# Performance work log

Hardware: AMD Instinct MI355X
Metric: run time of the kernel (lower is better)

## Reference

```python
import jax, jax.numpy as jnp
import numpy as np

N_NODES = 100000    # nodes in river network
N_PATHS = 1000000   # number of (src, dst) routing paths
MAX_DELAY = 16
DT = 1.0
CASCADE = 1.0
T = int(MAX_DELAY / DT)        # expanded time window (assert in original)
E = 8000000                    # total flattened path-node entries


def setup_inputs() -> dict:
    key = jax.random.key(0)
    k1, k2, k3 = jax.random.split(key, 3)
    params = jax.random.uniform(k1, (N_NODES,), dtype=jnp.float32)
    path_idxs = jnp.sort(jax.random.randint(k2, (E,), 0, N_PATHS, dtype=jnp.int32))
    path_nodes = jax.random.randint(k3, (E,), 0, N_NODES, dtype=jnp.int32)
    return {"params": params, "path_idxs": path_idxs, "path_nodes": path_nodes}


def reference(params, path_idxs, path_nodes):
    # irf_fn 'linear_storage': per-node linear-reservoir impulse response h(t)=exp(-t/k)/k
    k = params + 0.5                                  # storage const in [0.5, 1.5)
    t = jnp.arange(T, dtype=params.dtype) * DT        # [T]
    irfs = jnp.exp(-t[None, :] / k[:, None]) / k[:, None]   # [N, T]
    # frequency domain
    irfs_freq = jnp.fft.rfft(irfs, n=T, axis=-1)      # [N, F] complex
    # irf_agg 'log_triton': cascade-combine IRFs along each path = product of
    # transfer functions, done in log domain: gather logs, segment-sum per path.
    log_freq = jnp.log(irfs_freq)                     # [N, F] complex log
    gathered = log_freq[path_nodes]                   # [E, F] irregular gather
    agg_re = jax.ops.segment_sum(gathered.real, path_idxs, num_segments=N_PATHS)
    agg_im = jax.ops.segment_sum(gathered.imag, path_idxs, num_segments=N_PATHS)
    agg_log = (agg_re + 1j * agg_im) * CASCADE        # [P, F]
    irfs_freq_agg = jnp.exp(agg_log)
    # back to time domain
    irfs_agg = jnp.fft.irfft(irfs_freq_agg, n=T, axis=-1)   # [P, T]
    irfs_agg = jax.nn.relu(irfs_agg)
    irfs_agg = jnp.flip(irfs_agg, -1)                 # sampler.phi_k is identity for dt=1
    irfs_agg = irfs_agg / jnp.sum(irfs_agg, -1, keepdims=True)
    return irfs_agg                                   # COO values; coords scatter is a storage step
```

## Files before the change

### kernel.cpp

```cpp
#include <hip/hip_runtime.h>
#include <math.h>

#define N_NODES  100000
#define N_PATHS  1000000
#define E_TOT    8000000
#define NW_TOT   (E_TOT / 4)
#define NF       9
#define TAB_U32  25000
#define EB       1024
#define EPT      8
#define PB       256
#define KW       9

#define RMIN 0.135330f
#define RMAX 0.513420f
#define QSCALE (255.0f / (RMAX - RMIN))
#define DEQ    ((RMAX - RMIN) / 255.0f)

typedef int   v4i __attribute__((ext_vector_type(4)));
typedef float v4f __attribute__((ext_vector_type(4)));

__device__ __constant__ float COS16[16] = {
  1.0f,  0.92387953f,  0.70710678f,  0.38268343f,  0.0f, -0.38268343f, -0.70710678f, -0.92387953f,
 -1.0f, -0.92387953f, -0.70710678f, -0.38268343f,  0.0f,  0.38268343f,  0.70710678f,  0.92387953f };
__device__ __constant__ float SIN16[16] = {
  0.0f,  0.38268343f,  0.70710678f,  0.92387953f,  1.0f,  0.92387953f,  0.70710678f,  0.38268343f,
  0.0f, -0.38268343f, -0.70710678f, -0.92387953f, -1.0f, -0.92387953f, -0.70710678f, -0.38268343f };

__global__ void node_rq_kernel(const float* __restrict__ params,
                               unsigned char* __restrict__ rtab_q) {
    int n = blockIdx.x * blockDim.x + threadIdx.x;
    if (n >= N_NODES) return;
    float k = params[n] + 0.5f;
    float r = expf(-1.0f / k);
    float q = (r - RMIN) * QSCALE;
    q = fminf(fmaxf(q + 0.5f, 0.0f), 255.0f);
    rtab_q[n] = (unsigned char)q;
}

__device__ __forceinline__ void put_bounds(int a, int b, int e, int* __restrict__ start) {
    for (int p = a + 1; p <= b; ++p) start[p] = e;
}

__global__ __launch_bounds__(EB) void epass_kernel(const int* __restrict__ pidx,
                                                   const int* __restrict__ pnode,
                                                   const unsigned int* __restrict__ rtab_q,
                                                   int* __restrict__ start,
                                                   unsigned char* __restrict__ r8_all) {
    __shared__ unsigned int tab[TAB_U32];
    const unsigned char* tabb = (const unsigned char*)tab;
    int tid = threadIdx.x;
    for (int i = tid; i < TAB_U32; i += EB) tab[i] = rtab_q[i];
    __syncthreads();

    int base_q = blockIdx.x * EB * EPT;
#pragma unroll
    for (int g = 0; g < EPT; g++) {
        int q = base_q + g * EB + tid;
        if (q >= NW_TOT) break;
        int e = q * 4;
        v4i v = *((const v4i*)pidx + q);
        v4i w = *((const v4i*)pnode + q);
        uchar4 r;
        r.x = tabb[w.x];
        r.y = tabb[w.y];
        r.z = tabb[w.z];
        r.w = tabb[w.w];
        ((uchar4*)r8_all)[q] = r;
        int prev = __shfl_up((int)v.w, 1);
        if ((tid & 63) == 0) prev = (e == 0) ? -1 : pidx[e - 1];
        put_bounds(prev, v.x, e,     start);
        put_bounds(v.x,  v.y, e + 1, start);
        put_bounds(v.y,  v.z, e + 2, start);
        put_bounds(v.z,  v.w, e + 3, start);
        if (e + 4 == E_TOT) {
            for (int p = v.w + 1; p <= N_PATHS; ++p) start[p] = E_TOT;
        }
    }
}

__device__ __forceinline__ void quad_step(unsigned grp, int rem,
                                          float& d0, float& d8,
                                          float dr[7], float di[7]) {
    float ra = fmaf((float)(grp & 255u), DEQ, RMIN);
    float rb = (rem > 1) ? fmaf((float)((grp >> 8) & 255u), DEQ, RMIN) : 0.0f;
    float rc = (rem > 2) ? fmaf((float)((grp >> 16) & 255u), DEQ, RMIN) : 0.0f;
    float rd = (rem > 3) ? fmaf((float)(grp >> 24), DEQ, RMIN) : 0.0f;
    float sab = ra + rb, qab = ra * rb;
    float scd = rc + rd, qcd = rc * rd;
    float e1 = sab + scd;
    float e2 = fmaf(sab, scd, qab + qcd);
    float e3 = fmaf(qab, scd, qcd * sab);
    float e4 = qab * qcd;
#pragma unroll
    for (int f = 1; f <= 7; f++) {
        float tr = fmaf(-e1, COS16[f], 1.0f);
        tr = fmaf( e2, COS16[(2 * f) & 15], tr);
        tr = fmaf(-e3, COS16[(3 * f) & 15], tr);
        tr = fmaf( e4, COS16[(4 * f) & 15], tr);
        float ti = e1 * SIN16[f];
        ti = fmaf(-e2, SIN16[(2 * f) & 15], ti);
        ti = fmaf( e3, SIN16[(3 * f) & 15], ti);
        ti = fmaf(-e4, SIN16[(4 * f) & 15], ti);
        float a = dr[f - 1], b = di[f - 1];
        dr[f - 1] = fmaf(a, tr, -b * ti);
        di[f - 1] = fmaf(a, ti,  b * tr);
    }
    d0 *= ((1.0f - e1) + (e2 - e3)) + e4;
    d8 *= ((1.0f + e1) + (e2 + e3)) + e4;
}

__global__ __launch_bounds__(PB) void path_kernel(const int* __restrict__ start,
                                                  const unsigned int* __restrict__ r8w,
                                                  float* __restrict__ out) {
    int p = blockIdx.x * PB + threadIdx.x;
    if (p >= N_PATHS) return;

    int s0 = start[p];
    int s1 = start[p + 1];
    int len = s1 - s0;
    int nq = (len + 3) >> 2;
    int a0 = s0 >> 2;
    unsigned sh = (unsigned)(s0 & 3) * 8u;

    unsigned wv[KW];
#pragma unroll
    for (int i = 0; i < KW; ++i) {
        int idx = a0 + i;
        wv[i] = r8w[idx < NW_TOT ? idx : (NW_TOT - 1)];
    }

    float d0 = 1.0f, d8 = 1.0f;
    float dr[7], di[7];
#pragma unroll
    for (int f = 0; f < 7; f++) { dr[f] = 1.0f; di[f] = 0.0f; }

#pragma unroll
    for (int q = 0; q < KW - 1; ++q) {
        if (q < nq) {
            unsigned grp = (unsigned)((((unsigned long long)wv[q + 1] << 32) |
                                       (unsigned long long)wv[q]) >> sh);
            quad_step(grp, len - 4 * q, d0, d8, dr, di);
        }
    }
    if (nq > KW - 1) {
        unsigned cur = wv[KW - 1];
        for (int q = KW - 1; q < nq; ++q) {
            int w = a0 + q + 1;
            unsigned nxt = (w < NW_TOT) ? r8w[w] : 0u;
            unsigned grp = (unsigned)((((unsigned long long)nxt << 32) |
                                       (unsigned long long)cur) >> sh);
            cur = nxt;
            quad_step(grp, len - 4 * q, d0, d8, dr, di);
        }
    }

    float Xr[8], Xi[8];
    Xr[0] = 1.0f; Xi[0] = 0.0f;
#pragma unroll
    for (int f = 1; f < 8; f++) {
        float a = dr[f - 1], b = di[f - 1];
        float m = fmaf(a, a, b * b);
        float inv = d0 * __builtin_amdgcn_rcpf(m);
        Xr[f] =  a * inv;
        Xi[f] = -b * inv;
    }
    float X8 = d0 * __builtin_amdgcn_rcpf(d8);

    float xt[16];
    float c0 = 0.0f, c8 = 0.0f;
#pragma unroll
    for (int f = 1; f < 8; f++) {
        c0 += 2.0f * Xr[f];
        c8 += (f & 1) ? -2.0f * Xr[f] : 2.0f * Xr[f];
    }
    xt[0] = fmaxf((Xr[0] + X8 + c0) * (1.0f / 16.0f), 0.0f);
    xt[8] = fmaxf((Xr[0] + X8 + c8) * (1.0f / 16.0f), 0.0f);
    float ssum = xt[0] + xt[8];
#pragma unroll
    for (int t = 1; t < 8; t++) {
        float Ct = 0.0f, St = 0.0f;
#pragma unroll
        for (int f = 1; f < 8; f++) {
            int kk = (f * t) & 15;
            Ct = fmaf(2.0f * Xr[f], COS16[kk], Ct);
            St = fmaf(2.0f * Xi[f], SIN16[kk], St);
        }
        float base = Xr[0] + ((t & 1) ? -X8 : X8) + Ct;
        float xa = fmaxf((base - St) * (1.0f / 16.0f), 0.0f);
        float xb = fmaxf((base + St) * (1.0f / 16.0f), 0.0f);
        xt[t] = xa;
        xt[16 - t] = xb;
        ssum += xa + xb;
    }

    float invs = __builtin_amdgcn_rcpf(ssum);
    v4f* op4 = (v4f*)(out + (size_t)p * 16);
    op4[0] = (v4f){ xt[15] * invs, xt[14] * invs, xt[13] * invs, xt[12] * invs };
    op4[1] = (v4f){ xt[11] * invs, xt[10] * invs, xt[9]  * invs, xt[8]  * invs };
    op4[2] = (v4f){ xt[7]  * invs, xt[6]  * invs, xt[5]  * invs, xt[4]  * invs };
    op4[3] = (v4f){ xt[3]  * invs, xt[2]  * invs, xt[1]  * invs, xt[0]  * invs };
}

extern "C" void kernel_launch(void* const* d_in, const int* in_sizes, int n_in,
                              void* d_out, int out_size, void* d_ws, size_t ws_size,
                              hipStream_t stream) {
    const float* params = (const float*)d_in[0];
    const int* path_idxs = (const int*)d_in[1];
    const int* path_nodes = (const int*)d_in[2];
    float* out = (float*)d_out;

    size_t off_rq    = 0;
    size_t off_start = (off_rq + (size_t)N_NODES + 1023) & ~(size_t)1023;
    size_t off_r8    = (off_start + (size_t)(N_PATHS + 1) * 4 + 1023) & ~(size_t)1023;

    unsigned char* rtab_q = (unsigned char*)d_ws + off_rq;
    int* start = (int*)((char*)d_ws + off_start);
    unsigned char* r8_all = (unsigned char*)d_ws + off_r8;

    {
        int threads = 256;
        int blocks = (N_NODES + threads - 1) / threads;
        node_rq_kernel<<<blocks, threads, 0, stream>>>(params, rtab_q);
    }
    {
        int per_block = EB * EPT;
        int blocks = (NW_TOT + per_block - 1) / per_block;
        epass_kernel<<<blocks, EB, 0, stream>>>(path_idxs, path_nodes,
                                                (const unsigned int*)rtab_q,
                                                start, r8_all);
    }
    {
        int blocks = (N_PATHS + PB - 1) / PB;
        path_kernel<<<blocks, PB, 0, stream>>>(start, (const unsigned int*)r8_all, out);
    }
}
```

Before: 142.7 us.

## Split boundary and gather passes; process eight path nodes per polynomial step

The fused edge pass becomes two kernels. One computes path boundaries with 256-thread blocks and no shared-memory table. The other does the byte-table gather with a 1024-thread block and LDS. In the path kernel, the first 32 entries are now handled as octets: two quartic polynomials are combined into a degree-8 one before evaluating the 7 frequency bins. This halves the complex multiply-accumulates into the running product. The cost is an extra kernel launch, a second read pass, and more FMAs and registers per step, with some possible change in rounding.

```diff
diff --git a/kernel.cpp b/kernel.cpp
--- a/kernel.cpp
+++ b/kernel.cpp
@@ -5,10 +5,11 @@
 #define N_PATHS  1000000
 #define E_TOT    8000000
 #define NW_TOT   (E_TOT / 4)
-#define NF       9
 #define TAB_U32  25000
-#define EB       1024
-#define EPT      8
+#define BB       256
+#define BPT      8
+#define GB       1024
+#define GPT      8
 #define PB       256
 #define KW       9
 
@@ -19,6 +20,7 @@
 
 typedef int   v4i __attribute__((ext_vector_type(4)));
 typedef float v4f __attribute__((ext_vector_type(4)));
+typedef unsigned long long u64;
 
 __device__ __constant__ float COS16[16] = {
   1.0f,  0.92387953f,  0.70710678f,  0.38268343f,  0.0f, -0.38268343f, -0.70710678f, -0.92387953f,
@@ -42,31 +44,16 @@
     for (int p = a + 1; p <= b; ++p) start[p] = e;
 }
 
-__global__ __launch_bounds__(EB) void epass_kernel(const int* __restrict__ pidx,
-                                                   const int* __restrict__ pnode,
-                                                   const unsigned int* __restrict__ rtab_q,
-                                                   int* __restrict__ start,
-                                                   unsigned char* __restrict__ r8_all) {
-    __shared__ unsigned int tab[TAB_U32];
-    const unsigned char* tabb = (const unsigned char*)tab;
+__global__ __launch_bounds__(BB) void bound_kernel(const int* __restrict__ pidx,
+                                                   int* __restrict__ start) {
     int tid = threadIdx.x;
-    for (int i = tid; i < TAB_U32; i += EB) tab[i] = rtab_q[i];
-    __syncthreads();
-
-    int base_q = blockIdx.x * EB * EPT;
-#pragma unroll
-    for (int g = 0; g < EPT; g++) {
-        int q = base_q + g * EB + tid;
+    int base_q = blockIdx.x * BB * BPT;
+#pragma unroll
+    for (int g = 0; g < BPT; g++) {
+        int q = base_q + g * BB + tid;
         if (q >= NW_TOT) break;
         int e = q * 4;
         v4i v = *((const v4i*)pidx + q);
-        v4i w = *((const v4i*)pnode + q);
-        uchar4 r;
-        r.x = tabb[w.x];
-        r.y = tabb[w.y];
-        r.z = tabb[w.z];
-        r.w = tabb[w.w];
-        ((uchar4*)r8_all)[q] = r;
         int prev = __shfl_up((int)v.w, 1);
         if ((tid & 63) == 0) prev = (e == 0) ? -1 : pidx[e - 1];
         put_bounds(prev, v.x, e,     start);
@@ -76,6 +63,30 @@
         if (e + 4 == E_TOT) {
             for (int p = v.w + 1; p <= N_PATHS; ++p) start[p] = E_TOT;
         }
+    }
+}
+
+__global__ __launch_bounds__(GB) void gather_kernel(const int* __restrict__ pnode,
+                                                    const unsigned int* __restrict__ rtab_q,
+                                                    unsigned char* __restrict__ r8_all) {
+    __shared__ unsigned int tab[TAB_U32];
+    const unsigned char* tabb = (const unsigned char*)tab;
+    int tid = threadIdx.x;
+    for (int i = tid; i < TAB_U32; i += GB) tab[i] = rtab_q[i];
+    __syncthreads();
+
+    int base_q = blockIdx.x * GB * GPT;
+#pragma unroll
+    for (int g = 0; g < GPT; g++) {
+        int q = base_q + g * GB + tid;
+        if (q >= NW_TOT) break;
+        v4i w = *((const v4i*)pnode + q);
+        uchar4 r;
+        r.x = tabb[w.x];
+        r.y = tabb[w.y];
+        r.z = tabb[w.z];
+        r.w = tabb[w.w];
+        ((uchar4*)r8_all)[q] = r;
     }
 }
 
@@ -110,6 +121,65 @@
     d8 *= ((1.0f + e1) + (e2 + e3)) + e4;
 }
 
+__device__ __forceinline__ void oct_step(unsigned g0, unsigned g1, int rem,
+                                         float& d0, float& d8,
+                                         float dr[7], float di[7]) {
+    float r0 = fmaf((float)(g0 & 255u), DEQ, RMIN);
+    float r1 = (rem > 1) ? fmaf((float)((g0 >> 8) & 255u), DEQ, RMIN) : 0.0f;
+    float r2 = (rem > 2) ? fmaf((float)((g0 >> 16) & 255u), DEQ, RMIN) : 0.0f;
+    float r3 = (rem > 3) ? fmaf((float)(g0 >> 24), DEQ, RMIN) : 0.0f;
+    float r4 = (rem > 4) ? fmaf((float)(g1 & 255u), DEQ, RMIN) : 0.0f;
+    float r5 = (rem > 5) ? fmaf((float)((g1 >> 8) & 255u), DEQ, RMIN) : 0.0f;
+    float r6 = (rem > 6) ? fmaf((float)((g1 >> 16) & 255u), DEQ, RMIN) : 0.0f;
+    float r7 = (rem > 7) ? fmaf((float)(g1 >> 24), DEQ, RMIN) : 0.0f;
+    float sab = r0 + r1, qab = r0 * r1;
+    float scd = r2 + r3, qcd = r2 * r3;
+    float e1 = sab + scd;
+    float e2 = fmaf(sab, scd, qab + qcd);
+    float e3 = fmaf(qab, scd, qcd * sab);
+    float e4 = qab * qcd;
+    float sef = r4 + r5, qef = r4 * r5;
+    float sgh = r6 + r7, qgh = r6 * r7;
+    float f1 = sef + sgh;
+    float f2 = fmaf(sef, sgh, qef + qgh);
+    float f3 = fmaf(qef, sgh, qgh * sef);
+    float f4 = qef * qgh;
+    float c1 = e1 + f1;
+    float c2 = fmaf(e1, f1, e2 + f2);
+    float c3 = fmaf(e2, f1, fmaf(e1, f2, e3 + f3));
+    float c4 = fmaf(e3, f1, fmaf(e2, f2, fmaf(e1, f3, e4 + f4)));
+    float c5 = fmaf(e4, f1, fmaf(e3, f2, fmaf(e2, f3, e1 * f4)));
+    float c6 = fmaf(e4, f2, fmaf(e3, f3, e2 * f4));
+    float c7 = fmaf(e4, f3, e3 * f4);
+    float c8 = e4 * f4;
+#pragma unroll
+    for (int f = 1; f <= 7; f++) {
+        float tr = fmaf(-c1, COS16[f], 1.0f);
+        tr = fmaf( c2, COS16[(2 * f) & 15], tr);
+        tr = fmaf(-c3, COS16[(3 * f) & 15], tr);
+        tr = fmaf( c4, COS16[(4 * f) & 15], tr);
+        tr = fmaf(-c5, COS16[(5 * f) & 15], tr);
+        tr = fmaf( c6, COS16[(6 * f) & 15], tr);
+        tr = fmaf(-c7, COS16[(7 * f) & 15], tr);
+        tr = fmaf( c8, COS16[(8 * f) & 15], tr);
+        float ti = c1 * SIN16[f];
+        ti = fmaf(-c2, SIN16[(2 * f) & 15], ti);
+        ti = fmaf( c3, SIN16[(3 * f) & 15], ti);
+        ti = fmaf(-c4, SIN16[(4 * f) & 15], ti);
+        ti = fmaf( c5, SIN16[(5 * f) & 15], ti);
+        ti = fmaf(-c6, SIN16[(6 * f) & 15], ti);
+        ti = fmaf( c7, SIN16[(7 * f) & 15], ti);
+        ti = fmaf(-c8, SIN16[(8 * f) & 15], ti);
+        float a = dr[f - 1], b = di[f - 1];
+        dr[f - 1] = fmaf(a, tr, -b * ti);
+        di[f - 1] = fmaf(a, ti,  b * tr);
+    }
+    float ev = ((c2 + c4) + (c6 + c8));
+    float od = ((c1 + c3) + (c5 + c7));
+    d0 *= (1.0f + ev) - od;
+    d8 *= (1.0f + ev) + od;
+}
+
 __global__ __launch_bounds__(PB) void path_kernel(const int* __restrict__ start,
                                                   const unsigned int* __restrict__ r8w,
                                                   float* __restrict__ out) {
@@ -119,7 +189,7 @@
     int s0 = start[p];
     int s1 = start[p + 1];
     int len = s1 - s0;
-    int nq = (len + 3) >> 2;
+    int noct = (len + 7) >> 3;
     int a0 = s0 >> 2;
     unsigned sh = (unsigned)(s0 & 3) * 8u;
 
@@ -136,20 +206,21 @@
     for (int f = 0; f < 7; f++) { dr[f] = 1.0f; di[f] = 0.0f; }
 
 #pragma unroll
-    for (int q = 0; q < KW - 1; ++q) {
-        if (q < nq) {
-            unsigned grp = (unsigned)((((unsigned long long)wv[q + 1] << 32) |
-                                       (unsigned long long)wv[q]) >> sh);
-            quad_step(grp, len - 4 * q, d0, d8, dr, di);
+    for (int q = 0; q < 4; ++q) {
+        if (q < noct) {
+            u64 w01 = (((u64)wv[2 * q + 1]) << 32) | (u64)wv[2 * q];
+            u64 v = w01 >> sh;
+            if (sh) v |= ((u64)wv[2 * q + 2]) << (64u - sh);
+            oct_step((unsigned)v, (unsigned)(v >> 32), len - 8 * q, d0, d8, dr, di);
         }
     }
-    if (nq > KW - 1) {
+    if (len > 32) {
+        int nq = (len + 3) >> 2;
         unsigned cur = wv[KW - 1];
-        for (int q = KW - 1; q < nq; ++q) {
+        for (int q = 8; q < nq; ++q) {
             int w = a0 + q + 1;
             unsigned nxt = (w < NW_TOT) ? r8w[w] : 0u;
-            unsigned grp = (unsigned)((((unsigned long long)nxt << 32) |
-                                       (unsigned long long)cur) >> sh);
+            unsigned grp = (unsigned)((((u64)nxt << 32) | (u64)cur) >> sh);
             cur = nxt;
             quad_step(grp, len - 4 * q, d0, d8, dr, di);
         }
@@ -168,14 +239,14 @@
     float X8 = d0 * __builtin_amdgcn_rcpf(d8);
 
     float xt[16];
-    float c0 = 0.0f, c8 = 0.0f;
+    float c0 = 0.0f, c8s = 0.0f;
 #pragma unroll
     for (int f = 1; f < 8; f++) {
         c0 += 2.0f * Xr[f];
-        c8 += (f & 1) ? -2.0f * Xr[f] : 2.0f * Xr[f];
+        c8s += (f & 1) ? -2.0f * Xr[f] : 2.0f * Xr[f];
     }
     xt[0] = fmaxf((Xr[0] + X8 + c0) * (1.0f / 16.0f), 0.0f);
-    xt[8] = fmaxf((Xr[0] + X8 + c8) * (1.0f / 16.0f), 0.0f);
+    xt[8] = fmaxf((Xr[0] + X8 + c8s) * (1.0f / 16.0f), 0.0f);
     float ssum = xt[0] + xt[8];
 #pragma unroll
     for (int t = 1; t < 8; t++) {
@@ -224,11 +295,16 @@
         node_rq_kernel<<<blocks, threads, 0, stream>>>(params, rtab_q);
     }
     {
-        int per_block = EB * EPT;
+        int per_block = BB * BPT;
         int blocks = (NW_TOT + per_block - 1) / per_block;
-        epass_kernel<<<blocks, EB, 0, stream>>>(path_idxs, path_nodes,
-                                                (const unsigned int*)rtab_q,
-                                                start, r8_all);
+        bound_kernel<<<blocks, BB, 0, stream>>>(path_idxs, start);
+    }
+    {
+        int per_block = GB * GPT;
+        int blocks = (NW_TOT + per_block - 1) / per_block;
+        gather_kernel<<<blocks, GB, 0, stream>>>(path_nodes,
+                                                 (const unsigned int*)rtab_q,
+                                                 r8_all);
     }
     {
         int blocks = (N_PATHS + PB - 1) / PB;
```

After: 146.3 us. +2.5%, slower.
